# Kernel optimization log

Hardware: AMD Instinct MI355X
Metric: run time of the kernel (lower is better)

## Reference

```python
import jax, jax.numpy as jnp
import numpy as np

D_MODEL = 1024
NUM_HEADS = 16
HEAD_DIM = D_MODEL // NUM_HEADS
SCALE = HEAD_DIM ** -0.5


def setup_inputs() -> dict:
    key = jax.random.key(0)
    ks = jax.random.split(key, 5)
    B, N = 2, 2048
    x = jax.random.normal(ks[0], (B, N, D_MODEL), dtype=jnp.float32)
    # Linear params, torch layout: weight [out, in], bias [out]
    w_qkv = jax.random.normal(ks[1], (3 * D_MODEL, D_MODEL), dtype=jnp.float32) * (D_MODEL ** -0.5)
    b_qkv = jax.random.normal(ks[2], (3 * D_MODEL,), dtype=jnp.float32) * 0.02
    w_proj = jax.random.normal(ks[3], (D_MODEL, D_MODEL), dtype=jnp.float32) * (D_MODEL ** -0.5)
    b_proj = jax.random.normal(ks[4], (D_MODEL,), dtype=jnp.float32) * 0.02
    return {"x": x, "w_qkv": w_qkv, "b_qkv": b_qkv, "w_proj": w_proj, "b_proj": b_proj}


def reference(x, w_qkv, b_qkv, w_proj, b_proj):
    B, N, C = x.shape
    qkv = x @ w_qkv.T + b_qkv                      # [B, N, 3C]
    qkv = qkv.reshape(B, N, 3, NUM_HEADS, HEAD_DIM)
    qkv = jnp.transpose(qkv, (2, 0, 3, 1, 4))      # [3, B, H, N, d]
    q, k, v = qkv[0], qkv[1], qkv[2]
    attn = jnp.einsum('bhnd,bhmd->bhnm', q, k) * SCALE  # [B, H, N, N]
    attn = jax.nn.softmax(attn, axis=-1)
    # dropout is identity in eval mode
    out = jnp.einsum('bhnm,bhmd->bhnd', attn, v)   # [B, H, N, d]
    out = jnp.transpose(out, (0, 2, 1, 3)).reshape(B, N, C)
    return out @ w_proj.T + b_proj
```

## Files before the change

### kernel.cpp

```cpp
#include <hip/hip_runtime.h>

typedef short short8 __attribute__((ext_vector_type(8)));
typedef short short4v __attribute__((ext_vector_type(4)));
typedef float f32x4 __attribute__((ext_vector_type(4)));
typedef float float4v __attribute__((ext_vector_type(4)));
typedef int int4v __attribute__((ext_vector_type(4)));
typedef int int2v __attribute__((ext_vector_type(2)));

__device__ __forceinline__ short f2bf(float f) {
  union { float f; unsigned u; } v; v.f = f;
  unsigned r = v.u + 0x7FFFu + ((v.u >> 16) & 1u);
  return (short)(r >> 16);
}

__device__ __forceinline__ unsigned cvtpk_bf16(float lo, float hi) {
  unsigned r;
  asm("v_cvt_pk_bf16_f32 %0, %1, %2" : "=v"(r) : "v"(lo), "v"(hi));
  return r;
}

#define GLD16(gp, lp)                                                   \
  __builtin_amdgcn_global_load_lds(                                     \
      (const __attribute__((address_space(1))) void*)(gp),              \
      (__attribute__((address_space(3))) void*)(lp), 16, 0, 0)

#define QSCALE 0.18033688011112042f

__global__ __launch_bounds__(256) void cvt_all(
    const float* __restrict__ x, const float* __restrict__ wq, const float* __restrict__ wp,
    short* __restrict__ xb, short* __restrict__ wqb, short* __restrict__ wpb) {
  int i = blockIdx.x * 256 + threadIdx.x;
  const float* s; short* d; int off;
  if (i < 1048576)      { s = x;  d = xb;  off = i; }
  else if (i < 1835008) { s = wq; d = wqb; off = i - 1048576; }
  else                  { s = wp; d = wpb; off = i - 1835008; }
  float4v v = ((const float4v*)s)[off];
  short4v o;
  o.x = f2bf(v.x); o.y = f2bf(v.y); o.z = f2bf(v.z); o.w = f2bf(v.w);
  ((short4v*)d)[off] = o;
}

template <int MODE>
__global__ __launch_bounds__(256) void gemm_bt(
    const short* __restrict__ A, const short* __restrict__ Bw,
    const float* __restrict__ bias,
    short* __restrict__ qo, short* __restrict__ ko, short* __restrict__ vto,
    float* __restrict__ outf) {
  __shared__ short As[2][128 * 64];
  __shared__ short Bs[2][128 * 64];
  const int t = threadIdx.x;
  const int lane = t & 63, wid = t >> 6;
  const int g = lane >> 4, l15 = lane & 15;
  const int wr = (wid >> 1) * 64, wc = (wid & 1) * 64;
  const int bm0 = blockIdx.y * 128, bn0 = blockIdx.x * 128;

  const int sr = t >> 3;
  const int ssub0 = t & 7;

  const int swz = (l15 & 7) << 4;
  int aoff[2][4], boff[2][4];
#pragma unroll
  for (int kk = 0; kk < 2; ++kk)
#pragma unroll
    for (int f = 0; f < 4; ++f) {
      aoff[kk][f] = ((wr + f * 16 + l15) * 128 + kk * 64 + g * 16) ^ swz;
      boff[kk][f] = ((wc + f * 16 + l15) * 128 + kk * 64 + g * 16) ^ swz;
    }

  f32x4 acc[4][4] = {};

  auto stage = [&](int buf, int k0) {
#pragma unroll
    for (int i = 0; i < 4; ++i) {
      int row = i * 32 + sr;
      int s = ssub0 ^ (row & 7);
      char* ldsA = (char*)&As[buf][0] + (i * 256 + (t & ~63)) * 16;
      char* ldsB = (char*)&Bs[buf][0] + (i * 256 + (t & ~63)) * 16;
      GLD16(A + (size_t)(bm0 + row) * 1024 + k0 + s * 8, ldsA);
      GLD16(Bw + (size_t)(bn0 + row) * 1024 + k0 + s * 8, ldsB);
    }
  };

  stage(0, 0);
  stage(1, 64);
  int curOff = 0;

  for (int it = 0; it < 16; ++it) {
    if (it == 15) asm volatile("s_waitcnt vmcnt(0)" ::: "memory");
    else          asm volatile("s_waitcnt vmcnt(8)" ::: "memory");
    __builtin_amdgcn_s_barrier();
    __builtin_amdgcn_sched_barrier(0);
    const char* AsB = (const char*)&As[0][0] + curOff;
    const char* BsB = (const char*)&Bs[0][0] + curOff;
#pragma unroll
    for (int kk = 0; kk < 2; ++kk) {
      short8 a[4], b[4];
#pragma unroll
      for (int mi = 0; mi < 4; ++mi) a[mi] = *(const short8*)(AsB + aoff[kk][mi]);
#pragma unroll
      for (int ni = 0; ni < 4; ++ni) b[ni] = *(const short8*)(BsB + boff[kk][ni]);
#pragma unroll
      for (int mi = 0; mi < 4; ++mi)
#pragma unroll
        for (int ni = 0; ni < 4; ++ni)
          acc[mi][ni] = __builtin_amdgcn_mfma_f32_16x16x32_bf16(a[mi], b[ni], acc[mi][ni], 0, 0, 0);
    }
    __builtin_amdgcn_sched_barrier(0);
    __builtin_amdgcn_s_barrier();
    __builtin_amdgcn_sched_barrier(0);
    if (it + 2 < 16) stage(it & 1, (it + 2) * 64);
    curOff ^= 16384;
  }

  if constexpr (MODE == 0) {
    const int which = bn0 >> 10;
    if (which == 2) {
#pragma unroll
      for (int mi = 0; mi < 4; ++mi) {
#pragma unroll
        for (int ni = 0; ni < 4; ++ni) {
          int gcol = bn0 + wc + ni * 16 + l15;
          int w1 = gcol & 1023;
          int h = w1 >> 6, dd = w1 & 63;
          float bv = bias[gcol];
          int grow0 = bm0 + wr + mi * 16 + g * 4;
          int b_ = grow0 >> 11, n0 = grow0 & 2047;
          int bh = b_ * 16 + h;
          int nl = n0 & 63;
          int np = (n0 & ~63) | (nl & 32) | ((nl & 12) << 1) | ((nl & 16) >> 2);
          int2v pk;
          pk.x = (int)cvtpk_bf16(acc[mi][ni][0] + bv, acc[mi][ni][1] + bv);
          pk.y = (int)cvtpk_bf16(acc[mi][ni][2] + bv, acc[mi][ni][3] + bv);
          *(int2v*)(vto + ((size_t)bh * 64 + dd) * 2048 + np) = pk;
        }
      }
    } else {
      short* dst = (which == 0) ? qo : ko;
      const float sc = (which == 0) ? QSCALE : 1.0f;
#pragma unroll
      for (int mi = 0; mi < 4; ++mi) {
#pragma unroll
        for (int ni = 0; ni < 4; ++ni) {
          int gcol = bn0 + wc + ni * 16 + l15;
          int w1 = gcol & 1023;
          int h = w1 >> 6, dd = w1 & 63;
          float bv = bias[gcol];
#pragma unroll
          for (int r = 0; r < 4; ++r) {
            int grow = bm0 + wr + mi * 16 + g * 4 + r;
            int b_ = grow >> 11, n = grow & 2047;
            int bh = b_ * 16 + h;
            dst[((size_t)bh * 2048 + n) * 64 + dd] = f2bf((acc[mi][ni][r] + bv) * sc);
          }
        }
      }
    }
  } else {
#pragma unroll
    for (int mi = 0; mi < 4; ++mi) {
#pragma unroll
      for (int ni = 0; ni < 4; ++ni) {
        int gcol = bn0 + wc + ni * 16 + l15;
        float bv = bias[gcol];
#pragma unroll
        for (int r = 0; r < 4; ++r) {
          int grow = bm0 + wr + mi * 16 + g * 4 + r;
          outf[(size_t)grow * 1024 + gcol] = acc[mi][ni][r] + bv;
        }
      }
    }
  }
}

__global__ __launch_bounds__(256, 2) void attn_fused(
    const short* __restrict__ Qg, const short* __restrict__ Kg,
    const short* __restrict__ Vtg, short* __restrict__ AO) {
  __shared__ short Ks[2][64 * 64];
  __shared__ short Vs[2][64 * 64];
  const int bid = blockIdx.x;
  const int bh = bid & 31, qt = bid >> 5;
  const int t = threadIdx.x, wid = t >> 6, lane = t & 63;
  const int g = lane >> 4, l15 = lane & 15;
  const int q0w = qt * 128 + wid * 32;
  const short* qb = Qg + ((size_t)bh * 2048 + q0w) * 64;
  const short* kb = Kg + (size_t)bh * 2048 * 64;
  const short* vb = Vtg + (size_t)bh * 64 * 2048;

  const int srow = t >> 3;
  const int ssub = (t & 7) ^ (srow & 7);
  const short* ksrc0 = kb + srow * 64 + ssub * 8;
  const short* vsrc0 = vb + (size_t)srow * 2048 + ssub * 8;

  const int swz = (l15 & 7) << 4;
  int foff[2][4];
#pragma unroll
  for (int kk = 0; kk < 2; ++kk)
#pragma unroll
    for (int f = 0; f < 4; ++f)
      foff[kk][f] = ((f * 16 + l15) * 128 + kk * 64 + g * 16) ^ swz;

  short8 bq[2][2];
#pragma unroll
  for (int qf = 0; qf < 2; ++qf)
#pragma unroll
    for (int kk = 0; kk < 2; ++kk)
      bq[qf][kk] = *(const short8*)(qb + (qf * 16 + l15) * 64 + kk * 32 + g * 8);

#pragma unroll
  for (int i = 0; i < 2; ++i) {
    GLD16(ksrc0 + i * 32 * 64,           (char*)&Ks[0][0] + i * 4096 + wid * 1024);
    GLD16(vsrc0 + (size_t)i * 32 * 2048, (char*)&Vs[0][0] + i * 4096 + wid * 1024);
  }

  f32x4 acc[2][4] = {};
  float mrun[2] = {-3.0e38f, -3.0e38f}, lrun[2] = {0.f, 0.f};
  int curOff = 0;

  for (int it = 0; it < 32; ++it) {
    __syncthreads();
    if (it + 1 < 32) {
      const int n1 = (it + 1) * 64;
      char* ldsK = (char*)&Ks[(it + 1) & 1][0] + wid * 1024;
      char* ldsV = (char*)&Vs[(it + 1) & 1][0] + wid * 1024;
#pragma unroll
      for (int i = 0; i < 2; ++i) {
        GLD16(ksrc0 + (size_t)(n1 + i * 32) * 64, ldsK + i * 4096);
        GLD16(vsrc0 + (size_t)i * 32 * 2048 + n1, ldsV + i * 4096);
      }
    }
    const char* KsB = (const char*)&Ks[0][0] + curOff;
    const char* VsB = (const char*)&Vs[0][0] + curOff;
    curOff ^= 8192;

    f32x4 s[2][4] = {};
#pragma unroll
    for (int kk = 0; kk < 2; ++kk) {
      short8 ak[4];
#pragma unroll
      for (int kf = 0; kf < 4; ++kf) ak[kf] = *(const short8*)(KsB + foff[kk][kf]);
#pragma unroll
      for (int kf = 0; kf < 4; ++kf)
#pragma unroll
        for (int qf = 0; qf < 2; ++qf)
          s[qf][kf] = __builtin_amdgcn_mfma_f32_16x16x32_bf16(ak[kf], bq[qf][kk], s[qf][kf], 0, 0, 0);
    }

    float pm[2];
#pragma unroll
    for (int qf = 0; qf < 2; ++qf) {
      float m0 = fmaxf(s[qf][0][0], s[qf][0][1]);
      m0 = fmaxf(fmaxf(m0, s[qf][0][2]), s[qf][0][3]);
#pragma unroll
      for (int kf = 1; kf < 4; ++kf) {
        m0 = fmaxf(fmaxf(m0, s[qf][kf][0]), s[qf][kf][1]);
        m0 = fmaxf(fmaxf(m0, s[qf][kf][2]), s[qf][kf][3]);
      }
      float x = fmaxf(m0, __shfl_xor(m0, 16));
      pm[qf] = fmaxf(x, __shfl_xor(x, 32));
    }

    if (!__all((pm[0] - mrun[0] <= 8.f) && (pm[1] - mrun[1] <= 8.f))) {
#pragma unroll
      for (int qf = 0; qf < 2; ++qf) {
        float mn = fmaxf(mrun[qf], pm[qf]);
        float alpha = __builtin_amdgcn_exp2f(mrun[qf] - mn);
        mrun[qf] = mn;
        lrun[qf] *= alpha;
#pragma unroll
        for (int df = 0; df < 4; ++df)
#pragma unroll
          for (int r = 0; r < 4; ++r) acc[qf][df][r] *= alpha;
      }
    }

    unsigned wpk[2][4][2];
#pragma unroll
    for (int qf = 0; qf < 2; ++qf) {
      float rs = 0.f;
      float p[4][4];
#pragma unroll
      for (int kf = 0; kf < 4; ++kf)
#pragma unroll
        for (int r = 0; r < 4; ++r) {
          p[kf][r] = __builtin_amdgcn_exp2f(s[qf][kf][r] - mrun[qf]);
          rs += p[kf][r];
        }
      rs += __shfl_xor(rs, 16);
      rs += __shfl_xor(rs, 32);
      lrun[qf] += rs;
#pragma unroll
      for (int kf = 0; kf < 4; ++kf)
#pragma unroll
        for (int h = 0; h < 2; ++h)
          wpk[qf][kf][h] = cvtpk_bf16(p[kf][2 * h], p[kf][2 * h + 1]);
    }

#pragma unroll
    for (int kk = 0; kk < 2; ++kk) {
      short8 av[4];
#pragma unroll
      for (int df = 0; df < 4; ++df) av[df] = *(const short8*)(VsB + foff[kk][df]);
#pragma unroll
      for (int qf = 0; qf < 2; ++qf) {
        union { int4v i; short8 s; } pv;
        pv.i[0] = (int)wpk[qf][2 * kk][0];
        pv.i[1] = (int)wpk[qf][2 * kk][1];
        pv.i[2] = (int)wpk[qf][2 * kk + 1][0];
        pv.i[3] = (int)wpk[qf][2 * kk + 1][1];
#pragma unroll
        for (int df = 0; df < 4; ++df)
          acc[qf][df] = __builtin_amdgcn_mfma_f32_16x16x32_bf16(av[df], pv.s, acc[qf][df], 0, 0, 0);
      }
    }
  }

  const int b_ = bh >> 4, h = bh & 15;
#pragma unroll
  for (int qf = 0; qf < 2; ++qf) {
    const float inv = 1.0f / lrun[qf];
    short* outp = AO + ((size_t)b_ * 2048 + q0w + qf * 16 + l15) * 1024 + h * 64 + g * 4;
#pragma unroll
    for (int df = 0; df < 4; ++df) {
      short4v o;
#pragma unroll
      for (int r = 0; r < 4; ++r) o[r] = f2bf(acc[qf][df][r] * inv);
      *(short4v*)(outp + df * 16) = o;
    }
  }
}

extern "C" void kernel_launch(void* const* d_in, const int* in_sizes, int n_in,
                              void* d_out, int out_size, void* d_ws, size_t ws_size,
                              hipStream_t stream) {
  const float* x = (const float*)d_in[0];
  const float* w_qkv = (const float*)d_in[1];
  const float* b_qkv = (const float*)d_in[2];
  const float* w_proj = (const float*)d_in[3];
  const float* b_proj = (const float*)d_in[4];
  float* out = (float*)d_out;
  char* ws = (char*)d_ws;

  short* xb    = (short*)(ws + (size_t)0);
  short* wqkvb = (short*)(ws + ((size_t)8 << 20));
  short* wprojb= (short*)(ws + ((size_t)14 << 20));
  short* qb    = (short*)(ws + ((size_t)16 << 20));
  short* kb    = (short*)(ws + ((size_t)24 << 20));
  short* vtb   = (short*)(ws + ((size_t)32 << 20));
  short* aob   = (short*)(ws + ((size_t)40 << 20));

  cvt_all<<<8192, 256, 0, stream>>>(x, w_qkv, w_proj, xb, wqkvb, wprojb);
  gemm_bt<0><<<dim3(24, 32), 256, 0, stream>>>(xb, wqkvb, b_qkv, qb, kb, vtb, nullptr);
  attn_fused<<<512, 256, 0, stream>>>(qb, kb, vtb, aob);
  gemm_bt<1><<<dim3(8, 32), 256, 0, stream>>>(aob, wprojb, b_proj, nullptr, nullptr, nullptr, out);
}
```

Measured before the change: 123.2 us.

## Deepen attention K/V pipeline to 128-key stages with explicit vmcnt waits

```diff
diff --git a/kernel.cpp b/kernel.cpp
--- a/kernel.cpp
+++ b/kernel.cpp
@@ -175,8 +175,8 @@
 __global__ __launch_bounds__(256, 2) void attn_fused(
     const short* __restrict__ Qg, const short* __restrict__ Kg,
     const short* __restrict__ Vtg, short* __restrict__ AO) {
-  __shared__ short Ks[2][64 * 64];
-  __shared__ short Vs[2][64 * 64];
+  __shared__ short Ks[4][64 * 64];
+  __shared__ short Vs[4][64 * 64];
   const int bid = blockIdx.x;
   const int bh = bid & 31, qt = bid >> 5;
   const int t = threadIdx.x, wid = t >> 6, lane = t & 63;
@@ -206,112 +206,125 @@
     for (int kk = 0; kk < 2; ++kk)
       bq[qf][kk] = *(const short8*)(qb + (qf * 16 + l15) * 64 + kk * 32 + g * 8);
 
-#pragma unroll
-  for (int i = 0; i < 2; ++i) {
-    GLD16(ksrc0 + i * 32 * 64,           (char*)&Ks[0][0] + i * 4096 + wid * 1024);
-    GLD16(vsrc0 + (size_t)i * 32 * 2048, (char*)&Vs[0][0] + i * 4096 + wid * 1024);
-  }
+  auto stageP = [&](int buf, int p) {
+    const int n0 = p * 128;
+#pragma unroll
+    for (int sub = 0; sub < 2; ++sub) {
+      const int nn = n0 + sub * 64;
+      char* ldsK = (char*)&Ks[buf * 2 + sub][0] + wid * 1024;
+      char* ldsV = (char*)&Vs[buf * 2 + sub][0] + wid * 1024;
+#pragma unroll
+      for (int i = 0; i < 2; ++i) {
+        GLD16(ksrc0 + (size_t)(nn + i * 32) * 64, ldsK + i * 4096);
+        GLD16(vsrc0 + (size_t)i * 32 * 2048 + nn, ldsV + i * 4096);
+      }
+    }
+  };
+
+  stageP(0, 0);
+  stageP(1, 1);
 
   f32x4 acc[2][4] = {};
   float mrun[2] = {-3.0e38f, -3.0e38f}, lrun[2] = {0.f, 0.f};
-  int curOff = 0;
-
-  for (int it = 0; it < 32; ++it) {
-    __syncthreads();
-    if (it + 1 < 32) {
-      const int n1 = (it + 1) * 64;
-      char* ldsK = (char*)&Ks[(it + 1) & 1][0] + wid * 1024;
-      char* ldsV = (char*)&Vs[(it + 1) & 1][0] + wid * 1024;
-#pragma unroll
-      for (int i = 0; i < 2; ++i) {
-        GLD16(ksrc0 + (size_t)(n1 + i * 32) * 64, ldsK + i * 4096);
-        GLD16(vsrc0 + (size_t)i * 32 * 2048 + n1, ldsV + i * 4096);
-      }
-    }
-    const char* KsB = (const char*)&Ks[0][0] + curOff;
-    const char* VsB = (const char*)&Vs[0][0] + curOff;
-    curOff ^= 8192;
-
-    f32x4 s[2][4] = {};
-#pragma unroll
-    for (int kk = 0; kk < 2; ++kk) {
-      short8 ak[4];
-#pragma unroll
-      for (int kf = 0; kf < 4; ++kf) ak[kf] = *(const short8*)(KsB + foff[kk][kf]);
-#pragma unroll
-      for (int kf = 0; kf < 4; ++kf)
-#pragma unroll
-        for (int qf = 0; qf < 2; ++qf)
-          s[qf][kf] = __builtin_amdgcn_mfma_f32_16x16x32_bf16(ak[kf], bq[qf][kk], s[qf][kf], 0, 0, 0);
-    }
-
-    float pm[2];
-#pragma unroll
-    for (int qf = 0; qf < 2; ++qf) {
-      float m0 = fmaxf(s[qf][0][0], s[qf][0][1]);
-      m0 = fmaxf(fmaxf(m0, s[qf][0][2]), s[qf][0][3]);
-#pragma unroll
-      for (int kf = 1; kf < 4; ++kf) {
-        m0 = fmaxf(fmaxf(m0, s[qf][kf][0]), s[qf][kf][1]);
-        m0 = fmaxf(fmaxf(m0, s[qf][kf][2]), s[qf][kf][3]);
-      }
-      float x = fmaxf(m0, __shfl_xor(m0, 16));
-      pm[qf] = fmaxf(x, __shfl_xor(x, 32));
-    }
-
-    if (!__all((pm[0] - mrun[0] <= 8.f) && (pm[1] - mrun[1] <= 8.f))) {
+
+  for (int p = 0; p < 16; ++p) {
+    if (p == 15) asm volatile("s_waitcnt vmcnt(0)" ::: "memory");
+    else         asm volatile("s_waitcnt vmcnt(8)" ::: "memory");
+    __builtin_amdgcn_s_barrier();
+    __builtin_amdgcn_sched_barrier(0);
+    const int buf = p & 1;
+
+#pragma unroll
+    for (int sub = 0; sub < 2; ++sub) {
+      const char* KsB = (const char*)&Ks[buf * 2 + sub][0];
+      const char* VsB = (const char*)&Vs[buf * 2 + sub][0];
+
+      f32x4 s[2][4] = {};
+#pragma unroll
+      for (int kk = 0; kk < 2; ++kk) {
+        short8 ak[4];
+#pragma unroll
+        for (int kf = 0; kf < 4; ++kf) ak[kf] = *(const short8*)(KsB + foff[kk][kf]);
+#pragma unroll
+        for (int kf = 0; kf < 4; ++kf)
+#pragma unroll
+          for (int qf = 0; qf < 2; ++qf)
+            s[qf][kf] = __builtin_amdgcn_mfma_f32_16x16x32_bf16(ak[kf], bq[qf][kk], s[qf][kf], 0, 0, 0);
+      }
+
+      float pm[2];
 #pragma unroll
       for (int qf = 0; qf < 2; ++qf) {
-        float mn = fmaxf(mrun[qf], pm[qf]);
-        float alpha = __builtin_amdgcn_exp2f(mrun[qf] - mn);
-        mrun[qf] = mn;
-        lrun[qf] *= alpha;
-#pragma unroll
-        for (int df = 0; df < 4; ++df)
-#pragma unroll
-          for (int r = 0; r < 4; ++r) acc[qf][df][r] *= alpha;
-      }
-    }
-
-    unsigned wpk[2][4][2];
-#pragma unroll
-    for (int qf = 0; qf < 2; ++qf) {
-      float rs = 0.f;
-      float p[4][4];
-#pragma unroll
-      for (int kf = 0; kf < 4; ++kf)
-#pragma unroll
-        for (int r = 0; r < 4; ++r) {
-          p[kf][r] = __builtin_amdgcn_exp2f(s[qf][kf][r] - mrun[qf]);
-          rs += p[kf][r];
-        }
-      rs += __shfl_xor(rs, 16);
-      rs += __shfl_xor(rs, 32);
-      lrun[qf] += rs;
-#pragma unroll
-      for (int kf = 0; kf < 4; ++kf)
-#pragma unroll
-        for (int h = 0; h < 2; ++h)
-          wpk[qf][kf][h] = cvtpk_bf16(p[kf][2 * h], p[kf][2 * h + 1]);
-    }
-
-#pragma unroll
-    for (int kk = 0; kk < 2; ++kk) {
-      short8 av[4];
-#pragma unroll
-      for (int df = 0; df < 4; ++df) av[df] = *(const short8*)(VsB + foff[kk][df]);
+        float m0 = fmaxf(s[qf][0][0], s[qf][0][1]);
+        m0 = fmaxf(fmaxf(m0, s[qf][0][2]), s[qf][0][3]);
+#pragma unroll
+        for (int kf = 1; kf < 4; ++kf) {
+          m0 = fmaxf(fmaxf(m0, s[qf][kf][0]), s[qf][kf][1]);
+          m0 = fmaxf(fmaxf(m0, s[qf][kf][2]), s[qf][kf][3]);
+        }
+        float x = fmaxf(m0, __shfl_xor(m0, 16));
+        pm[qf] = fmaxf(x, __shfl_xor(x, 32));
+      }
+
+      if (!__all((pm[0] - mrun[0] <= 8.f) && (pm[1] - mrun[1] <= 8.f))) {
+#pragma unroll
+        for (int qf = 0; qf < 2; ++qf) {
+          float mn = fmaxf(mrun[qf], pm[qf]);
+          float alpha = __builtin_amdgcn_exp2f(mrun[qf] - mn);
+          mrun[qf] = mn;
+          lrun[qf] *= alpha;
+#pragma unroll
+          for (int df = 0; df < 4; ++df)
+#pragma unroll
+            for (int r = 0; r < 4; ++r) acc[qf][df][r] *= alpha;
+        }
+      }
+
+      unsigned wpk[2][4][2];
 #pragma unroll
       for (int qf = 0; qf < 2; ++qf) {
-        union { int4v i; short8 s; } pv;
-        pv.i[0] = (int)wpk[qf][2 * kk][0];
-        pv.i[1] = (int)wpk[qf][2 * kk][1];
-        pv.i[2] = (int)wpk[qf][2 * kk + 1][0];
-        pv.i[3] = (int)wpk[qf][2 * kk + 1][1];
-#pragma unroll
-        for (int df = 0; df < 4; ++df)
-          acc[qf][df] = __builtin_amdgcn_mfma_f32_16x16x32_bf16(av[df], pv.s, acc[qf][df], 0, 0, 0);
-      }
-    }
+        float rs = 0.f;
+        float pp[4][4];
+#pragma unroll
+        for (int kf = 0; kf < 4; ++kf)
+#pragma unroll
+          for (int r = 0; r < 4; ++r) {
+            pp[kf][r] = __builtin_amdgcn_exp2f(s[qf][kf][r] - mrun[qf]);
+            rs += pp[kf][r];
+          }
+        rs += __shfl_xor(rs, 16);
+        rs += __shfl_xor(rs, 32);
+        lrun[qf] += rs;
+#pragma unroll
+        for (int kf = 0; kf < 4; ++kf)
+#pragma unroll
+          for (int h = 0; h < 2; ++h)
+            wpk[qf][kf][h] = cvtpk_bf16(pp[kf][2 * h], pp[kf][2 * h + 1]);
+      }
+
+#pragma unroll
+      for (int kk = 0; kk < 2; ++kk) {
+        short8 av[4];
+#pragma unroll
+        for (int df = 0; df < 4; ++df) av[df] = *(const short8*)(VsB + foff[kk][df]);
+#pragma unroll
+        for (int qf = 0; qf < 2; ++qf) {
+          union { int4v i; short8 s; } pv;
+          pv.i[0] = (int)wpk[qf][2 * kk][0];
+          pv.i[1] = (int)wpk[qf][2 * kk][1];
+          pv.i[2] = (int)wpk[qf][2 * kk + 1][0];
+          pv.i[3] = (int)wpk[qf][2 * kk + 1][1];
+#pragma unroll
+          for (int df = 0; df < 4; ++df)
+            acc[qf][df] = __builtin_amdgcn_mfma_f32_16x16x32_bf16(av[df], pv.s, acc[qf][df], 0, 0, 0);
+        }
+      }
+    }
+
+    __builtin_amdgcn_sched_barrier(0);
+    __builtin_amdgcn_s_barrier();
+    __builtin_amdgcn_sched_barrier(0);
+    if (p + 2 < 16) stageP(buf, p + 2);
   }
 
   const int b_ = bh >> 4, h = bh & 15;
```

New measurement: 122.4 us. About the same (-0.7%).
